# Kernel optimization log

Hardware: AMD Instinct MI355X
Metric: run time of the kernel (lower is better)

Reference implementation:

```python
import jax, jax.numpy as jnp
import numpy as np

NUM_FEATURES = 35
BLANK = 2          # local blank index inside each 3-way category
NEG = -1e30        # finite stand-in for -inf (keeps grads NaN-free)


def _ctc_losses(log_probs, ext, skip_ok, valid, input_lengths, target_lengths):
    """Batched CTC negative log-likelihood.
    log_probs: [T,B,F,3] log-softmax per category
    ext:       [B,F,L] extended label sequence (blank interleaved), L=2S+1
    skip_ok:   [B,F,L] whether the l-2 transition is allowed
    valid:     [B,F,L] positions within 2*target_len+1
    Returns per-(B,F) loss.
    """
    T = log_probs.shape[0]

    emit0 = jnp.take_along_axis(log_probs[0], ext, axis=-1)  # [B,F,L]
    alpha = jnp.full_like(emit0, NEG)
    alpha = alpha.at[..., 0].set(emit0[..., 0])
    alpha = alpha.at[..., 1].set(jnp.where(target_lengths > 0, emit0[..., 1], NEG))

    pad1 = jnp.full(alpha.shape[:-1] + (1,), NEG, alpha.dtype)
    pad2 = jnp.full(alpha.shape[:-1] + (2,), NEG, alpha.dtype)

    def step(alpha, xs):
        lp_t, t = xs                                   # lp_t: [B,F,3]
        emit = jnp.take_along_axis(lp_t, ext, axis=-1)  # [B,F,L]
        a1 = jnp.concatenate([pad1, alpha[..., :-1]], axis=-1)
        a2 = jnp.concatenate([pad2, alpha[..., :-2]], axis=-1)
        prev = jnp.logaddexp(jnp.logaddexp(alpha, a1),
                             jnp.where(skip_ok, a2, NEG))
        new = jnp.where(valid, prev + emit, NEG)
        active = (t < input_lengths)[:, None, None]     # [B,1,1]
        return jnp.where(active, new, alpha), None

    alpha, _ = jax.lax.scan(step, alpha, (log_probs[1:], jnp.arange(1, T)))

    idx_last = 2 * target_lengths                       # [B,F] final blank
    last = jnp.take_along_axis(alpha, idx_last[..., None], axis=-1)[..., 0]
    prev_ = jnp.take_along_axis(alpha, jnp.maximum(idx_last - 1, 0)[..., None], axis=-1)[..., 0]
    prev_ = jnp.where(target_lengths > 0, prev_, NEG)
    ll = jnp.logaddexp(last, prev_)
    # zero_infinity=True: impossible alignments contribute 0 loss
    return jnp.where(ll > -1e29, -ll, 0.0)


def reference(logits, targets, input_lengths, target_lengths):
    # logits: [T,B,71]; targets: [B,35,S] local labels in {0,1};
    # input_lengths: [B]; target_lengths: [B,35]
    T, B, _ = logits.shape
    F = NUM_FEATURES
    pos = logits[:, :, :F]
    neg = logits[:, :, F:2 * F]
    blank = jnp.broadcast_to(logits[:, :, 2 * F:2 * F + 1], pos.shape)
    lp = jax.nn.log_softmax(jnp.stack([pos, neg, blank], axis=-1), axis=-1)  # [T,B,F,3]

    S = targets.shape[-1]
    L = 2 * S + 1
    ext = jnp.full((B, F, L), BLANK, jnp.int32).at[:, :, 1::2].set(targets.astype(jnp.int32))
    posL = jnp.arange(L)
    valid = posL[None, None, :] < (2 * target_lengths[..., None] + 1)
    ext_m2 = jnp.pad(ext[:, :, :-2], ((0, 0), (0, 0), (2, 0)), constant_values=BLANK)
    skip_ok = (ext != BLANK) & (ext != ext_m2) & (posL[None, None, :] >= 2)

    loss_bf = _ctc_losses(lp, ext, skip_ok, valid, input_lengths, target_lengths)  # [B,F]
    # reduction='mean': per-sample loss divided by its target length, averaged over batch,
    # then summed over the 35 feature categories (the python loop accumulates per-feature means)
    tl = jnp.maximum(target_lengths, 1).astype(loss_bf.dtype)
    return jnp.sum(jnp.mean(loss_bf / tl, axis=0))


def setup_inputs() -> dict:
    T, B, S = 600, 32, 80
    key = jax.random.key(0)
    k1, k2, k3 = jax.random.split(key, 3)
    logits = jax.random.normal(k1, (T, B, 2 * NUM_FEATURES + 1), dtype=jnp.float32)
    targets = jax.random.randint(k2, (B, NUM_FEATURES, S), 0, 2, dtype=jnp.int32)
    target_lengths = jax.random.randint(k3, (B, NUM_FEATURES), 40, S + 1, dtype=jnp.int32)
    input_lengths = jnp.full((B,), T, dtype=jnp.int32)
    return {"logits": logits, "targets": targets,
            "input_lengths": input_lengths, "target_lengths": target_lengths}
```

## Files before the change

### kernel.cpp

```cpp
#include <hip/hip_runtime.h>

#define LN2 0.6931471805599453f

typedef float f32x4 __attribute__((ext_vector_type(4)));

__device__ __forceinline__ float dpp_shr1_zero(float x) {
    return __int_as_float(__builtin_amdgcn_update_dpp(
        0, __float_as_int(x), 0x138, 0xF, 0xF, true));
}
__device__ __forceinline__ int dpp_shr1_keep(int x) {
    return __builtin_amdgcn_update_dpp(x, x, 0x138, 0xF, 0xF, false);
}
__device__ __forceinline__ float dpp_shl1_zero(float x) {
    return __int_as_float(__builtin_amdgcn_update_dpp(
        0, __float_as_int(x), 0x130, 0xF, 0xF, true));
}
__device__ __forceinline__ int dpp_shl1_keep(int x) {
    return __builtin_amdgcn_update_dpp(x, x, 0x130, 0xF, 0xF, false);
}
__device__ __forceinline__ float exp2i_clamped(int d) {
    int k = 127 + d;
    k = (k < 1) ? 1 : ((k > 254) ? 254 : k);
    return __uint_as_float(((unsigned)k) << 23);
}
__device__ __forceinline__ float sel3(int e, float v0, float v1, float v2) {
    return (e == 2) ? v2 : ((e == 1) ? v1 : v0);
}

struct FwdState {
    float a0, a1, a2;
    float s1, k0, k1;
    int   esum;
};
struct BwdState {
    float c0, c1, c2;
    float s1b, kA, kB;
    int   esum;
};

__device__ __forceinline__ void fwd_step(float em0, float em1, float em2,
                                         FwdState& st, float skm2) {
    float d2 = dpp_shr1_zero(st.a2);
    float d1 = dpp_shr1_zero(st.a1);
    float n0 = fmaf(st.k0, d1, fmaf(st.s1, d2, st.a0)) * em0;
    float n1 = fmaf(st.k1, d2, st.a1 + st.a0) * em1;
    float n2 = fmaf(skm2, st.a0, st.a2 + st.a1) * em2;
    st.a0 = n0; st.a1 = n1; st.a2 = n2;
}
__device__ __forceinline__ void bwd_step(float em0, float em1, float em2,
                                         BwdState& st, float skm2) {
    float d3 = dpp_shl1_zero(st.c0);
    float d4 = dpp_shl1_zero(st.c1);
    float n0 = fmaf(skm2, st.c2, st.c0 + st.c1) * em0;
    float n1 = fmaf(st.kA, d3, st.c1 + st.c2) * em1;
    float n2 = fmaf(st.kB, d4, fmaf(st.s1b, d3, st.c2)) * em2;
    st.c0 = n0; st.c1 = n1; st.c2 = n2;
}

__device__ __forceinline__ void fwd_rescale(FwdState& st, float skm0, float skm1) {
    float m = fmaxf(fmaxf(st.a0, st.a1), st.a2);
    int ebits = (int)(__float_as_uint(m) >> 23);
    bool dead = (ebits == 0);
    int de = dead ? 0 : (127 - ebits);
    float scz = dead ? 0.0f : exp2i_clamped(de);
    st.a0 *= scz; st.a1 *= scz; st.a2 *= scz;
    st.esum -= de;
    #pragma unroll
    for (int r = 0; r < 5; ++r) {
        int en = dpp_shr1_keep(st.esum);
        st.esum = dead ? en : st.esum;
    }
    int enf = dpp_shr1_keep(st.esum);
    int gap = enf - st.esum;
    int adj = (gap > 64) ? (gap - 64) : 0;
    float sc3 = exp2i_clamped(-adj);
    st.a0 *= sc3; st.a1 *= sc3; st.a2 *= sc3;
    st.esum += adj;
    st.s1 = exp2i_clamped(gap - adj);
    st.k0 = skm0 * st.s1;
    st.k1 = skm1 * st.s1;
}
__device__ __forceinline__ void bwd_rescale(BwdState& st, float sknA, float sknB) {
    float m = fmaxf(fmaxf(st.c0, st.c1), st.c2);
    int ebits = (int)(__float_as_uint(m) >> 23);
    bool dead = (ebits == 0);
    int de = dead ? 0 : (127 - ebits);
    float scz = dead ? 0.0f : exp2i_clamped(de);
    st.c0 *= scz; st.c1 *= scz; st.c2 *= scz;
    st.esum -= de;
    #pragma unroll
    for (int r = 0; r < 5; ++r) {
        int en = dpp_shl1_keep(st.esum);
        st.esum = dead ? en : st.esum;
    }
    #pragma unroll
    for (int r = 0; r < 3; ++r) {
        int enl = dpp_shr1_keep(st.esum);
        int mn = (enl < st.esum) ? enl : st.esum;
        st.esum = dead ? mn : st.esum;
    }
    int deadR = dpp_shl1_keep(dead ? 1 : 0);
    int enf = dpp_shl1_keep(st.esum);
    int gap = enf - st.esum;
    int adj = (gap > 64) ? (gap - 64) : 0;
    adj = (adj > 126) ? 126 : adj;
    adj = deadR ? 0 : adj;
    float sc3 = exp2i_clamped(-adj);
    st.c0 *= sc3; st.c1 *= sc3; st.c2 *= sc3;
    st.esum += adj;
    float s1b = exp2i_clamped(gap - adj);
    st.s1b = deadR ? 0.f : s1b;
    st.kA = sknA * st.s1b;
    st.kB = sknB * st.s1b;
}

__global__ __launch_bounds__(128, 1) void ctc_kernel(
    const float* __restrict__ logits,
    const int* __restrict__ targets,
    const int* __restrict__ input_lengths,
    const int* __restrict__ target_lengths,
    float* __restrict__ loss_out,
    int T, int B, int Ff, int S)
{
    const int p = blockIdx.x;
    const int b = p / Ff;
    const int f = p - b * Ff;
    const int tid = (int)threadIdx.x;
    const int wid = tid >> 6;
    const int lane = tid & 63;
    const int C = 2 * Ff + 1;
    const int L = 2 * S + 1;

    const int tl = target_lengths[p];
    const int il = input_lengths[b];
    const int tbase = p * S;

    int e0i, e1i, e2i;
    float skm0, skm1, skm2;
    {
        int e[3]; float sk[3];
        const int l0 = 3 * lane;
        #pragma unroll
        for (int j = 0; j < 3; ++j) {
            int l = l0 + j;
            int ev = 2; float sok = 0.f;
            if (l < L && (l & 1)) {
                int s = (l - 1) >> 1;
                ev = targets[tbase + s];
                if (s >= 1) sok = (targets[tbase + s - 1] != ev) ? 1.f : 0.f;
            }
            e[j] = ev; sk[j] = sok;
        }
        e0i = e[0]; e1i = e[1]; e2i = e[2];
        skm0 = sk[0]; skm1 = sk[1]; skm2 = sk[2];
    }
    const float sknA = dpp_shl1_zero(skm0);
    const float sknB = dpp_shl1_zero(skm1);

    __shared__ f32x4 slp[640];
    {
        const float* lg = logits + (size_t)b * C;
        const size_t strideT = (size_t)B * C;
        float c0 = 0.f, c1 = 0.f, c2 = 0.f;
        if (tid < T) {
            const float* r = lg + (size_t)tid * strideT;
            c0 = r[f]; c1 = r[Ff + f]; c2 = r[2 * Ff];
        }
        #pragma unroll 1
        for (int j = 0; j < 5; ++j) {
            int i = tid + (j << 7);
            int inx = i + 128;
            float n0 = 0.f, n1 = 0.f, n2 = 0.f;
            if (inx < T) {
                const float* r = lg + (size_t)inx * strideT;
                n0 = r[f]; n1 = r[Ff + f]; n2 = r[2 * Ff];
            }
            f32x4 v = {0.f, 0.f, 0.f, 0.f};
            if (i < T) {
                float m = fmaxf(fmaxf(c0, c1), c2);
                float ep = __expf(c0 - m);
                float en = __expf(c1 - m);
                float eb = __expf(c2 - m);
                float inv = __builtin_amdgcn_rcpf(ep + en + eb);
                v[0] = ep * inv; v[1] = en * inv; v[2] = eb * inv;
            }
            if (i < 640) slp[i] = v;
            c0 = n0; c1 = n1; c2 = n2;
        }
    }
    __syncthreads();

    const char* base8 = (const char*)slp;
    const char* qt0 = base8 + (e0i << 2);
    const char* qt1 = base8 + (e1i << 2);
    const char* qt2 = base8 + (e2i << 2);

    const int TL = (il < T) ? il : T;
    const int m_ = (TL >= 2) ? ((TL - 1) >> 1) : 0;
    const int Fn = m_;
    const int Bk = (TL >= 2) ? (TL - 2 - m_) : 0;

    __shared__ float sa[192];
    __shared__ float sg[194];
    __shared__ int   seb[65];
    __shared__ float sdot[64];
    __shared__ int   sE[64];

    FwdState fs;
    fs.a0 = 0.f; fs.a1 = 0.f; fs.a2 = 0.f; fs.s1 = 1.f;
    fs.k0 = skm0; fs.k1 = skm1; fs.esum = 0;

    if (wid == 0) {
        {
            f32x4 E0 = slp[0];
            fs.a0 = (lane == 0) ? E0[2] : 0.f;
            fs.a1 = (lane == 0 && tl > 0) ? sel3(e1i, E0[0], E0[1], E0[2]) : 0.f;
            fs.a2 = 0.f;
        }
        const int t_endF = Fn + 1;
        const char* pr0 = qt0 + 16;
        const char* pr1 = qt1 + 16;
        const char* pr2 = qt2 + 16;
#define LDE(OFF, E) { E[0] = *(const float*)(pr0 + (OFF)); \
                      E[1] = *(const float*)(pr1 + (OFF)); \
                      E[2] = *(const float*)(pr2 + (OFF)); }
        float A0[3], A1[3], A2[3], A3[3], B0[3], B1[3], B2[3], B3[3];
        float C0[3], C1[3], C2[3], C3[3], D0[3], D1[3], D2[3], D3[3];
        int t = 1;
        if (t + 15 < t_endF) {
            LDE(  0, A0); LDE( 16, A1); LDE( 32, A2); LDE( 48, A3);
            LDE( 64, B0); LDE( 80, B1); LDE( 96, B2); LDE(112, B3);
            LDE(128, C0); LDE(144, C1); LDE(160, C2); LDE(176, C3);
            LDE(192, D0); LDE(208, D1); LDE(224, D2); LDE(240, D3);
        }
        #pragma unroll 1
        for (; t + 15 < t_endF; t += 16) {
            fwd_rescale(fs, skm0, skm1);
            fwd_step(A0[0], A0[1], A0[2], fs, skm2);
            fwd_step(A1[0], A1[1], A1[2], fs, skm2);
            fwd_step(A2[0], A2[1], A2[2], fs, skm2);
            fwd_step(A3[0], A3[1], A3[2], fs, skm2);
            LDE(256, A0); LDE(272, A1); LDE(288, A2); LDE(304, A3);
            fwd_step(B0[0], B0[1], B0[2], fs, skm2);
            fwd_step(B1[0], B1[1], B1[2], fs, skm2);
            fwd_step(B2[0], B2[1], B2[2], fs, skm2);
            fwd_step(B3[0], B3[1], B3[2], fs, skm2);
            LDE(320, B0); LDE(336, B1); LDE(352, B2); LDE(368, B3);
            fwd_rescale(fs, skm0, skm1);
            fwd_step(C0[0], C0[1], C0[2], fs, skm2);
            fwd_step(C1[0], C1[1], C1[2], fs, skm2);
            fwd_step(C2[0], C2[1], C2[2], fs, skm2);
            fwd_step(C3[0], C3[1], C3[2], fs, skm2);
            LDE(384, C0); LDE(400, C1); LDE(416, C2); LDE(432, C3);
            fwd_step(D0[0], D0[1], D0[2], fs, skm2);
            fwd_step(D1[0], D1[1], D1[2], fs, skm2);
            fwd_step(D2[0], D2[1], D2[2], fs, skm2);
            fwd_step(D3[0], D3[1], D3[2], fs, skm2);
            LDE(448, D0); LDE(464, D1); LDE(480, D2); LDE(496, D3);
            pr0 += 256; pr1 += 256; pr2 += 256;
        }
#undef LDE
        #pragma unroll 1
        for (; t < t_endF; ++t) {
            int o = t << 4;
            float e0 = *(const float*)(qt0 + o);
            float e1 = *(const float*)(qt1 + o);
            float e2 = *(const float*)(qt2 + o);
            fwd_step(e0, e1, e2, fs, skm2);
        }
        {
            int l = 3 * lane;
            sa[l] = fs.a0; sa[l + 1] = fs.a1; sa[l + 2] = fs.a2;
        }
    } else {
        BwdState bs;
        {
            int oTL = (TL - 1) << 4;
            float eL0 = *(const float*)(qt0 + oTL);
            float eL1 = *(const float*)(qt1 + oTL);
            float eL2 = *(const float*)(qt2 + oTL);
            int l0i = 3 * lane;
            int end1 = 2 * tl, end2 = 2 * tl - 1;
            bs.c0 = (l0i == end1 || l0i == end2) ? eL0 : 0.f;
            bs.c1 = (l0i + 1 == end1 || l0i + 1 == end2) ? eL1 : 0.f;
            bs.c2 = (l0i + 2 == end1 || l0i + 2 == end2) ? eL2 : 0.f;
            bs.s1b = 1.f; bs.kA = sknA; bs.kB = sknB;
            bs.esum = 0;
        }
        const char* pb0 = qt0 + ((TL - 2) << 4);
        const char* pb1 = qt1 + ((TL - 2) << 4);
        const char* pb2 = qt2 + ((TL - 2) << 4);
#define LDB(OFF, E) { E[0] = *(const float*)(pb0 - (OFF)); \
                      E[1] = *(const float*)(pb1 - (OFF)); \
                      E[2] = *(const float*)(pb2 - (OFF)); }
        float GA0[3], GA1[3], GA2[3], GA3[3], GB0[3], GB1[3], GB2[3], GB3[3];
        float GC0[3], GC1[3], GC2[3], GC3[3], GD0[3], GD1[3], GD2[3], GD3[3];
        int k = 0;
        if (k + 15 < Bk) {
            LDB(  0, GA0); LDB( 16, GA1); LDB( 32, GA2); LDB( 48, GA3);
            LDB( 64, GB0); LDB( 80, GB1); LDB( 96, GB2); LDB(112, GB3);
            LDB(128, GC0); LDB(144, GC1); LDB(160, GC2); LDB(176, GC3);
            LDB(192, GD0); LDB(208, GD1); LDB(224, GD2); LDB(240, GD3);
        }
        #pragma unroll 1
        for (; k + 15 < Bk; k += 16) {
            bwd_rescale(bs, sknA, sknB);
            bwd_step(GA0[0], GA0[1], GA0[2], bs, skm2);
            bwd_step(GA1[0], GA1[1], GA1[2], bs, skm2);
            bwd_step(GA2[0], GA2[1], GA2[2], bs, skm2);
            bwd_step(GA3[0], GA3[1], GA3[2], bs, skm2);
            LDB(256, GA0); LDB(272, GA1); LDB(288, GA2); LDB(304, GA3);
            bwd_step(GB0[0], GB0[1], GB0[2], bs, skm2);
            bwd_step(GB1[0], GB1[1], GB1[2], bs, skm2);
            bwd_step(GB2[0], GB2[1], GB2[2], bs, skm2);
            bwd_step(GB3[0], GB3[1], GB3[2], bs, skm2);
            LDB(320, GB0); LDB(336, GB1); LDB(352, GB2); LDB(368, GB3);
            bwd_rescale(bs, sknA, sknB);
            bwd_step(GC0[0], GC0[1], GC0[2], bs, skm2);
            bwd_step(GC1[0], GC1[1], GC1[2], bs, skm2);
            bwd_step(GC2[0], GC2[1], GC2[2], bs, skm2);
            bwd_step(GC3[0], GC3[1], GC3[2], bs, skm2);
            LDB(384, GC0); LDB(400, GC1); LDB(416, GC2); LDB(432, GC3);
            bwd_step(GD0[0], GD0[1], GD0[2], bs, skm2);
            bwd_step(GD1[0], GD1[1], GD1[2], bs, skm2);
            bwd_step(GD2[0], GD2[1], GD2[2], bs, skm2);
            bwd_step(GD3[0], GD3[1], GD3[2], bs, skm2);
            LDB(448, GD0); LDB(464, GD1); LDB(480, GD2); LDB(496, GD3);
            pb0 -= 256; pb1 -= 256; pb2 -= 256;
        }
#undef LDB
        int trow = TL - 2 - k;
        #pragma unroll 1
        for (; trow >= m_ + 1; --trow) {
            int o = trow << 4;
            float g0 = *(const float*)(qt0 + o);
            float g1 = *(const float*)(qt1 + o);
            float g2 = *(const float*)(qt2 + o);
            bwd_step(g0, g1, g2, bs, skm2);
        }
        {
            int l = 3 * lane;
            sg[l] = bs.c0; sg[l + 1] = bs.c1; sg[l + 2] = bs.c2;
            seb[lane] = bs.esum;
            if (lane == 0) { sg[192] = 0.f; sg[193] = 0.f; seb[64] = 0; }
        }
    }
    __syncthreads();

    if (wid == 0) {
        int eB = seb[lane];
        float scn = exp2i_clamped(seb[lane + 1] - eB);
        float g0 = sg[3 * lane], g1 = sg[3 * lane + 1], g2 = sg[3 * lane + 2];
        float g3 = sg[3 * lane + 3] * scn;
        float g4 = sg[3 * lane + 4] * scn;
        float s0 = fmaf(skm2, g2, g0 + g1);
        float s1 = fmaf(sknA, g3, g1 + g2);
        float s2 = fmaf(sknB, g4, g2 + g3);
        float dot = fs.a0 * s0 + fs.a1 * s1 + fs.a2 * s2;
        sdot[lane] = dot;
        sE[lane] = fs.esum + eB;
    }
    __syncthreads();
    if (tid == 0) {
        float loss = 0.f;
        if (TL == 1) {
            float v = sa[2 * tl] + ((tl > 0) ? sa[2 * tl - 1] : 0.f);
            if (v > 0.f) loss = -(__log2f(v) * LN2);
        } else {
            int Emax = -0x40000000;
            for (int i = 0; i < 64; ++i)
                if (sdot[i] > 0.f && sE[i] > Emax) Emax = sE[i];
            if (Emax != -0x40000000) {
                float sum = 0.f;
                for (int i = 0; i < 64; ++i) {
                    int d = sE[i] - Emax;
                    if (d > -127 && sdot[i] > 0.f) sum += sdot[i] * exp2i_clamped(d);
                }
                loss = -((__log2f(sum) + (float)Emax) * LN2);
            }
        }
        float denom = (tl > 0) ? (float)tl : 1.0f;
        loss_out[p] = loss / denom;
    }
}

__global__ __launch_bounds__(256) void reduce_kernel(
    const float* __restrict__ v, float* __restrict__ out, int n, float invB)
{
    __shared__ float buf[256];
    float s = 0.f;
    for (int i = (int)threadIdx.x; i < n; i += 256) s += v[i];
    buf[threadIdx.x] = s;
    __syncthreads();
    for (int off = 128; off > 0; off >>= 1) {
        if ((int)threadIdx.x < off) buf[threadIdx.x] += buf[threadIdx.x + off];
        __syncthreads();
    }
    if (threadIdx.x == 0) out[0] = buf[0] * invB;
}

extern "C" void kernel_launch(void* const* d_in, const int* in_sizes, int n_in,
                              void* d_out, int out_size, void* d_ws, size_t ws_size,
                              hipStream_t stream) {
    const float* logits         = (const float*)d_in[0];
    const int*   targets        = (const int*)d_in[1];
    const int*   input_lengths  = (const int*)d_in[2];
    const int*   target_lengths = (const int*)d_in[3];
    float* out = (float*)d_out;

    const int B  = in_sizes[2];
    const int BF = in_sizes[3];
    const int Ff = BF / B;
    const int S  = in_sizes[1] / BF;
    const int C  = 2 * Ff + 1;
    const int T  = in_sizes[0] / (B * C);

    float* losses = (float*)d_ws;

    ctc_kernel<<<BF, 128, 0, stream>>>(logits, targets, input_lengths,
                                       target_lengths, losses, T, B, Ff, S);
    reduce_kernel<<<1, 256, 0, stream>>>(losses, out, BF, 1.0f / (float)B);
}
```

Measured before the change: 53.01 us.

## Replace per-lane gathered LDS loads with broadcast vector load plus FMA label select

The softmax stage now stores the probabilities re-encoded as differences (p1-p0, p0-pb, pb). Each lane reads one shared float4 per time step as a broadcast and rebuilds its three emission values with FMAs driven by float target labels and lane parity. This replaces three per-lane scattered LDS loads per step and drops the hand-written 16-deep register prefetch pipeline. It trades LDS traffic and register pressure for a few extra VALU ops per step on the serial recurrence, with slightly different float rounding.

```diff
diff --git a/kernel.cpp b/kernel.cpp
--- a/kernel.cpp
+++ b/kernel.cpp
@@ -22,9 +22,6 @@
     int k = 127 + d;
     k = (k < 1) ? 1 : ((k > 254) ? 254 : k);
     return __uint_as_float(((unsigned)k) << 23);
-}
-__device__ __forceinline__ float sel3(int e, float v0, float v1, float v2) {
-    return (e == 2) ? v2 : ((e == 1) ? v1 : v0);
 }
 
 struct FwdState {
@@ -135,27 +132,29 @@
     const int il = input_lengths[b];
     const int tbase = p * S;
 
-    int e0i, e1i, e2i;
-    float skm0, skm1, skm2;
+    float tf0, tf1, tf2, skm0, skm1, skm2;
     {
-        int e[3]; float sk[3];
+        float tf[3], sk[3];
         const int l0 = 3 * lane;
         #pragma unroll
         for (int j = 0; j < 3; ++j) {
             int l = l0 + j;
-            int ev = 2; float sok = 0.f;
+            float tv = 0.f, sok = 0.f;
             if (l < L && (l & 1)) {
                 int s = (l - 1) >> 1;
-                ev = targets[tbase + s];
+                int ev = targets[tbase + s];
+                tv = (float)ev;
                 if (s >= 1) sok = (targets[tbase + s - 1] != ev) ? 1.f : 0.f;
             }
-            e[j] = ev; sk[j] = sok;
-        }
-        e0i = e[0]; e1i = e[1]; e2i = e[2];
+            tf[j] = tv; sk[j] = sok;
+        }
+        tf0 = tf[0]; tf1 = tf[1]; tf2 = tf[2];
         skm0 = sk[0]; skm1 = sk[1]; skm2 = sk[2];
     }
     const float sknA = dpp_shl1_zero(skm0);
     const float sknB = dpp_shl1_zero(skm1);
+    const float vP = (float)(lane & 1);
+    const float vQ = 1.0f - vP;
 
     __shared__ f32x4 slp[640];
     {
@@ -182,18 +181,14 @@
                 float en = __expf(c1 - m);
                 float eb = __expf(c2 - m);
                 float inv = __builtin_amdgcn_rcpf(ep + en + eb);
-                v[0] = ep * inv; v[1] = en * inv; v[2] = eb * inv;
+                float p0 = ep * inv, p1 = en * inv, pb = eb * inv;
+                v[0] = p1 - p0; v[1] = p0 - pb; v[2] = pb;
             }
             if (i < 640) slp[i] = v;
             c0 = n0; c1 = n1; c2 = n2;
         }
     }
     __syncthreads();
-
-    const char* base8 = (const char*)slp;
-    const char* qt0 = base8 + (e0i << 2);
-    const char* qt1 = base8 + (e1i << 2);
-    const char* qt2 = base8 + (e2i << 2);
 
     const int TL = (il < T) ? il : T;
     const int m_ = (TL >= 2) ? ((TL - 1) >> 1) : 0;
@@ -206,6 +201,13 @@
     __shared__ float sdot[64];
     __shared__ int   sE[64];
 
+#define EMF(E, EV0, EV1, EV2) \
+    float iA = fmaf(vP, (E)[1], (E)[2]); \
+    float iB = fmaf(vQ, (E)[1], (E)[2]); \
+    float EV0 = fmaf(tf0, (E)[0], iA); \
+    float EV1 = fmaf(tf1, (E)[0], iB); \
+    float EV2 = fmaf(tf2, (E)[0], iA);
+
     FwdState fs;
     fs.a0 = 0.f; fs.a1 = 0.f; fs.a2 = 0.f; fs.s1 = 1.f;
     fs.k0 = skm0; fs.k1 = skm1; fs.esum = 0;
@@ -213,61 +215,27 @@
     if (wid == 0) {
         {
             f32x4 E0 = slp[0];
+            float e1i0 = fmaf(tf1, E0[0], E0[1] + E0[2]);
             fs.a0 = (lane == 0) ? E0[2] : 0.f;
-            fs.a1 = (lane == 0 && tl > 0) ? sel3(e1i, E0[0], E0[1], E0[2]) : 0.f;
+            fs.a1 = (lane == 0 && tl > 0) ? e1i0 : 0.f;
             fs.a2 = 0.f;
         }
         const int t_endF = Fn + 1;
-        const char* pr0 = qt0 + 16;
-        const char* pr1 = qt1 + 16;
-        const char* pr2 = qt2 + 16;
-#define LDE(OFF, E) { E[0] = *(const float*)(pr0 + (OFF)); \
-                      E[1] = *(const float*)(pr1 + (OFF)); \
-                      E[2] = *(const float*)(pr2 + (OFF)); }
-        float A0[3], A1[3], A2[3], A3[3], B0[3], B1[3], B2[3], B3[3];
-        float C0[3], C1[3], C2[3], C3[3], D0[3], D1[3], D2[3], D3[3];
         int t = 1;
-        if (t + 15 < t_endF) {
-            LDE(  0, A0); LDE( 16, A1); LDE( 32, A2); LDE( 48, A3);
-            LDE( 64, B0); LDE( 80, B1); LDE( 96, B2); LDE(112, B3);
-            LDE(128, C0); LDE(144, C1); LDE(160, C2); LDE(176, C3);
-            LDE(192, D0); LDE(208, D1); LDE(224, D2); LDE(240, D3);
-        }
-        #pragma unroll 1
-        for (; t + 15 < t_endF; t += 16) {
+#define FSTEP(IDX) { f32x4 E = slp[(IDX)]; EMF(E, e0, e1, e2) \
+                     fwd_step(e0, e1, e2, fs, skm2); }
+        #pragma unroll 1
+        for (; t + 16 <= t_endF; t += 16) {
             fwd_rescale(fs, skm0, skm1);
-            fwd_step(A0[0], A0[1], A0[2], fs, skm2);
-            fwd_step(A1[0], A1[1], A1[2], fs, skm2);
-            fwd_step(A2[0], A2[1], A2[2], fs, skm2);
-            fwd_step(A3[0], A3[1], A3[2], fs, skm2);
-            LDE(256, A0); LDE(272, A1); LDE(288, A2); LDE(304, A3);
-            fwd_step(B0[0], B0[1], B0[2], fs, skm2);
-            fwd_step(B1[0], B1[1], B1[2], fs, skm2);
-            fwd_step(B2[0], B2[1], B2[2], fs, skm2);
-            fwd_step(B3[0], B3[1], B3[2], fs, skm2);
-            LDE(320, B0); LDE(336, B1); LDE(352, B2); LDE(368, B3);
+            FSTEP(t)      FSTEP(t + 1)  FSTEP(t + 2)  FSTEP(t + 3)
+            FSTEP(t + 4)  FSTEP(t + 5)  FSTEP(t + 6)  FSTEP(t + 7)
             fwd_rescale(fs, skm0, skm1);
-            fwd_step(C0[0], C0[1], C0[2], fs, skm2);
-            fwd_step(C1[0], C1[1], C1[2], fs, skm2);
-            fwd_step(C2[0], C2[1], C2[2], fs, skm2);
-            fwd_step(C3[0], C3[1], C3[2], fs, skm2);
-            LDE(384, C0); LDE(400, C1); LDE(416, C2); LDE(432, C3);
-            fwd_step(D0[0], D0[1], D0[2], fs, skm2);
-            fwd_step(D1[0], D1[1], D1[2], fs, skm2);
-            fwd_step(D2[0], D2[1], D2[2], fs, skm2);
-            fwd_step(D3[0], D3[1], D3[2], fs, skm2);
-            LDE(448, D0); LDE(464, D1); LDE(480, D2); LDE(496, D3);
-            pr0 += 256; pr1 += 256; pr2 += 256;
-        }
-#undef LDE
-        #pragma unroll 1
-        for (; t < t_endF; ++t) {
-            int o = t << 4;
-            float e0 = *(const float*)(qt0 + o);
-            float e1 = *(const float*)(qt1 + o);
-            float e2 = *(const float*)(qt2 + o);
-            fwd_step(e0, e1, e2, fs, skm2);
-        }
+            FSTEP(t + 8)  FSTEP(t + 9)  FSTEP(t + 10) FSTEP(t + 11)
+            FSTEP(t + 12) FSTEP(t + 13) FSTEP(t + 14) FSTEP(t + 15)
+        }
+        #pragma unroll 1
+        for (; t < t_endF; ++t) FSTEP(t)
+#undef FSTEP
         {
             int l = 3 * lane;
             sa[l] = fs.a0; sa[l + 1] = fs.a1; sa[l + 2] = fs.a2;
@@ -275,10 +243,8 @@
     } else {
         BwdState bs;
         {
-            int oTL = (TL - 1) << 4;
-            float eL0 = *(const float*)(qt0 + oTL);
-            float eL1 = *(const float*)(qt1 + oTL);
-            float eL2 = *(const float*)(qt2 + oTL);
+            f32x4 EL = slp[TL - 1];
+            EMF(EL, eL0, eL1, eL2)
             int l0i = 3 * lane;
             int end1 = 2 * tl, end2 = 2 * tl - 1;
             bs.c0 = (l0i == end1 || l0i == end2) ? eL0 : 0.f;
@@ -287,57 +253,22 @@
             bs.s1b = 1.f; bs.kA = sknA; bs.kB = sknB;
             bs.esum = 0;
         }
-        const char* pb0 = qt0 + ((TL - 2) << 4);
-        const char* pb1 = qt1 + ((TL - 2) << 4);
-        const char* pb2 = qt2 + ((TL - 2) << 4);
-#define LDB(OFF, E) { E[0] = *(const float*)(pb0 - (OFF)); \
-                      E[1] = *(const float*)(pb1 - (OFF)); \
-                      E[2] = *(const float*)(pb2 - (OFF)); }
-        float GA0[3], GA1[3], GA2[3], GA3[3], GB0[3], GB1[3], GB2[3], GB3[3];
-        float GC0[3], GC1[3], GC2[3], GC3[3], GD0[3], GD1[3], GD2[3], GD3[3];
         int k = 0;
-        if (k + 15 < Bk) {
-            LDB(  0, GA0); LDB( 16, GA1); LDB( 32, GA2); LDB( 48, GA3);
-            LDB( 64, GB0); LDB( 80, GB1); LDB( 96, GB2); LDB(112, GB3);
-            LDB(128, GC0); LDB(144, GC1); LDB(160, GC2); LDB(176, GC3);
-            LDB(192, GD0); LDB(208, GD1); LDB(224, GD2); LDB(240, GD3);
-        }
-        #pragma unroll 1
-        for (; k + 15 < Bk; k += 16) {
+        int tr = TL - 2;
+#define BSTEP(IDX) { f32x4 E = slp[(IDX)]; EMF(E, e0, e1, e2) \
+                     bwd_step(e0, e1, e2, bs, skm2); }
+        #pragma unroll 1
+        for (; k + 16 <= Bk; k += 16, tr -= 16) {
             bwd_rescale(bs, sknA, sknB);
-            bwd_step(GA0[0], GA0[1], GA0[2], bs, skm2);
-            bwd_step(GA1[0], GA1[1], GA1[2], bs, skm2);
-            bwd_step(GA2[0], GA2[1], GA2[2], bs, skm2);
-            bwd_step(GA3[0], GA3[1], GA3[2], bs, skm2);
-            LDB(256, GA0); LDB(272, GA1); LDB(288, GA2); LDB(304, GA3);
-            bwd_step(GB0[0], GB0[1], GB0[2], bs, skm2);
-            bwd_step(GB1[0], GB1[1], GB1[2], bs, skm2);
-            bwd_step(GB2[0], GB2[1], GB2[2], bs, skm2);
-            bwd_step(GB3[0], GB3[1], GB3[2], bs, skm2);
-            LDB(320, GB0); LDB(336, GB1); LDB(352, GB2); LDB(368, GB3);
+            BSTEP(tr)      BSTEP(tr - 1)  BSTEP(tr - 2)  BSTEP(tr - 3)
+            BSTEP(tr - 4)  BSTEP(tr - 5)  BSTEP(tr - 6)  BSTEP(tr - 7)
             bwd_rescale(bs, sknA, sknB);
-            bwd_step(GC0[0], GC0[1], GC0[2], bs, skm2);
-            bwd_step(GC1[0], GC1[1], GC1[2], bs, skm2);
-            bwd_step(GC2[0], GC2[1], GC2[2], bs, skm2);
-            bwd_step(GC3[0], GC3[1], GC3[2], bs, skm2);
-            LDB(384, GC0); LDB(400, GC1); LDB(416, GC2); LDB(432, GC3);
-            bwd_step(GD0[0], GD0[1], GD0[2], bs, skm2);
-            bwd_step(GD1[0], GD1[1], GD1[2], bs, skm2);
-            bwd_step(GD2[0], GD2[1], GD2[2], bs, skm2);
-            bwd_step(GD3[0], GD3[1], GD3[2], bs, skm2);
-            LDB(448, GD0); LDB(464, GD1); LDB(480, GD2); LDB(496, GD3);
-            pb0 -= 256; pb1 -= 256; pb2 -= 256;
-        }
-#undef LDB
-        int trow = TL - 2 - k;
-        #pragma unroll 1
-        for (; trow >= m_ + 1; --trow) {
-            int o = trow << 4;
-            float g0 = *(const float*)(qt0 + o);
-            float g1 = *(const float*)(qt1 + o);
-            float g2 = *(const float*)(qt2 + o);
-            bwd_step(g0, g1, g2, bs, skm2);
-        }
+            BSTEP(tr - 8)  BSTEP(tr - 9)  BSTEP(tr - 10) BSTEP(tr - 11)
+            BSTEP(tr - 12) BSTEP(tr - 13) BSTEP(tr - 14) BSTEP(tr - 15)
+        }
+        #pragma unroll 1
+        for (; k < Bk; ++k, --tr) BSTEP(tr)
+#undef BSTEP
         {
             int l = 3 * lane;
             sg[l] = bs.c0; sg[l + 1] = bs.c1; sg[l + 2] = bs.c2;
@@ -354,9 +285,9 @@
         float g3 = sg[3 * lane + 3] * scn;
         float g4 = sg[3 * lane + 4] * scn;
         float s0 = fmaf(skm2, g2, g0 + g1);
-        float s1 = fmaf(sknA, g3, g1 + g2);
-        float s2 = fmaf(sknB, g4, g2 + g3);
-        float dot = fs.a0 * s0 + fs.a1 * s1 + fs.a2 * s2;
+        float s1v = fmaf(sknA, g3, g1 + g2);
+        float s2v = fmaf(sknB, g4, g2 + g3);
+        float dot = fs.a0 * s0 + fs.a1 * s1v + fs.a2 * s2v;
         sdot[lane] = dot;
         sE[lane] = fs.esum + eB;
     }
@@ -382,6 +313,7 @@
         float denom = (tl > 0) ? (float)tl : 1.0f;
         loss_out[p] = loss / denom;
     }
+#undef EMF
 }
 
 __global__ __launch_bounds__(256) void reduce_kernel(
```

After: 60.42 us. +14.0%, slower.
